# Optimization experiments

Hardware: AMD Instinct MI355X
Metric: run time of the kernel (lower is better)

The kernel has to match this reference:

```python
import jax, jax.numpy as jnp
import numpy as np

N_TOKENS = 1_000_000
NUM_FEATURES = 128
NUM_CLUSTERS = 64


def setup_inputs() -> dict:
    key = jax.random.key(0)
    kx, kc = jax.random.split(key)
    x = jax.random.normal(kx, (1, N_TOKENS, NUM_FEATURES), dtype=jnp.float32)
    # learned parameter, initialized as torch.randn(num_clusters, num_features)
    cluster_centers = jax.random.normal(kc, (NUM_CLUSTERS, NUM_FEATURES), dtype=jnp.float32)
    return {"x": x, "cluster_centers": cluster_centers}


def reference(x, cluster_centers):
    # x: (1, n, d); cluster_centers: (k, d)
    # O(n*k*d) broadcast intermediate of the original). argmin is identical
    # to argmin over torch.norm since sqrt is monotone.
    x2 = jnp.sum(x * x, axis=-1)                                  # (1, n)
    c2 = jnp.sum(cluster_centers * cluster_centers, axis=-1)      # (k,)
    xc = jnp.einsum('bnd,kd->bnk', x, cluster_centers)            # (1, n, k)
    d2 = x2[..., None] + c2[None, None, :] - 2.0 * xc             # (1, n, k)
    # nearest token index for each cluster (min over the token dim)
    indices = jnp.argmin(d2, axis=1)                              # (1, k)
    # gather the selected token features: (1, k, d)
    selected = x[:, indices[0], :]
    return selected
```

## Files before the change

### kernel.cpp

```cpp
#include <hip/hip_runtime.h>
#include <math.h>

#define NTOK   1000000
#define NFEAT  128
#define NCLUS  64
#define TT     256
#define KC     32
#define XPAD   260
#define NTILES ((NTOK + TT - 1) / TT)

__global__ __launch_bounds__(256, 3)
void cluster_part_kernel(const float* __restrict__ x, const float* __restrict__ cc,
                         float* __restrict__ pv, int* __restrict__ pi)
{
    __shared__ float xs[KC][XPAD];
    __shared__ float cs[KC][NCLUS];
    __shared__ float x2s[TT];
    __shared__ float c2s[NCLUS];

    const int tid = threadIdx.x;
    const int cg  = tid & 7;
    const int tg  = tid >> 3;
    const int l   = tid & 3;
    const int g   = tid >> 2;

    const int  tile = blockIdx.x;
    const long tb   = (long)tile * TT;

    float acc[8][8];
    #pragma unroll
    for (int i = 0; i < 8; ++i)
        #pragma unroll
        for (int j = 0; j < 8; ++j) acc[i][j] = 0.f;

    for (int kc = 0; kc < NFEAT / KC; ++kc) {
        __syncthreads();

        {
            const float* src = cc + (long)g * NFEAT + kc * KC + l * 4;
            float4 a = *(const float4*)(src);
            float4 b = *(const float4*)(src + 16);
            cs[l*4+0][g] = a.x; cs[l*4+1][g] = a.y;
            cs[l*4+2][g] = a.z; cs[l*4+3][g] = a.w;
            cs[16+l*4+0][g] = b.x; cs[16+l*4+1][g] = b.y;
            cs[16+l*4+2][g] = b.z; cs[16+l*4+3][g] = b.w;
            float s = 0.f;
            s = fmaf(a.x, a.x, s); s = fmaf(a.y, a.y, s);
            s = fmaf(a.z, a.z, s); s = fmaf(a.w, a.w, s);
            s = fmaf(b.x, b.x, s); s = fmaf(b.y, b.y, s);
            s = fmaf(b.z, b.z, s); s = fmaf(b.w, b.w, s);
            s += __shfl_xor(s, 1);
            s += __shfl_xor(s, 2);
            if (l == 0) { if (kc == 0) c2s[g] = s; else c2s[g] += s; }
        }

        #pragma unroll
        for (int r = 0; r < 4; ++r) {
            const int  row = r * 64 + g;
            long n = tb + row;
            if (n > NTOK - 1) n = NTOK - 1;
            const float* src = x + n * NFEAT + kc * KC + l * 4;
            float4 a = *(const float4*)(src);
            float4 b = *(const float4*)(src + 16);
            xs[l*4+0][row] = a.x; xs[l*4+1][row] = a.y;
            xs[l*4+2][row] = a.z; xs[l*4+3][row] = a.w;
            xs[16+l*4+0][row] = b.x; xs[16+l*4+1][row] = b.y;
            xs[16+l*4+2][row] = b.z; xs[16+l*4+3][row] = b.w;
            float s = 0.f;
            s = fmaf(a.x, a.x, s); s = fmaf(a.y, a.y, s);
            s = fmaf(a.z, a.z, s); s = fmaf(a.w, a.w, s);
            s = fmaf(b.x, b.x, s); s = fmaf(b.y, b.y, s);
            s = fmaf(b.z, b.z, s); s = fmaf(b.w, b.w, s);
            s += __shfl_xor(s, 1);
            s += __shfl_xor(s, 2);
            if (l == 0) { if (kc == 0) x2s[row] = s; else x2s[row] += s; }
        }
        __syncthreads();

        #pragma unroll 2
        for (int k = 0; k < KC; ++k) {
            float4 xa = *(const float4*)&xs[k][tg * 8];
            float4 xb = *(const float4*)&xs[k][tg * 8 + 4];
            float4 ca = *(const float4*)&cs[k][cg * 8];
            float4 cb = *(const float4*)&cs[k][cg * 8 + 4];
            float xv[8] = {xa.x, xa.y, xa.z, xa.w, xb.x, xb.y, xb.z, xb.w};
            float cv[8] = {ca.x, ca.y, ca.z, ca.w, cb.x, cb.y, cb.z, cb.w};
            #pragma unroll
            for (int i = 0; i < 8; ++i)
                #pragma unroll
                for (int j = 0; j < 8; ++j)
                    acc[i][j] = fmaf(xv[i], cv[j], acc[i][j]);
        }
    }

    float bestv[8]; int besti[8];
    #pragma unroll
    for (int j = 0; j < 8; ++j) { bestv[j] = INFINITY; besti[j] = 0; }

    float c2r[8];
    #pragma unroll
    for (int j = 0; j < 8; ++j) c2r[j] = c2s[cg * 8 + j];

    #pragma unroll
    for (int i = 0; i < 8; ++i) {
        const long n = tb + tg * 8 + i;
        if (n >= NTOK) continue;
        const float x2 = x2s[tg * 8 + i];
        #pragma unroll
        for (int j = 0; j < 8; ++j) {
            float s = (x2 + c2r[j]) - 2.0f * acc[i][j];
            if (s < bestv[j]) { bestv[j] = s; besti[j] = (int)n; }
        }
    }

    __syncthreads();
    float* rv = &xs[0][0];
    int*   ri = (int*)&cs[0][0];
    #pragma unroll
    for (int j = 0; j < 8; ++j) {
        rv[(cg * 8 + j) * 32 + tg] = bestv[j];
        ri[(cg * 8 + j) * 32 + tg] = besti[j];
    }
    __syncthreads();
    if (tid < NCLUS) {
        float bv = rv[tid * 32]; int bi = ri[tid * 32];
        #pragma unroll
        for (int t = 1; t < 32; ++t) {
            float v = rv[tid * 32 + t]; int ii = ri[tid * 32 + t];
            if (v < bv || (v == bv && ii < bi)) { bv = v; bi = ii; }
        }
        pv[(long)tile * NCLUS + tid] = bv;
        pi[(long)tile * NCLUS + tid] = bi;
    }
}

__global__ __launch_bounds__(256)
void cluster_final_kernel(const float* __restrict__ x,
                          const float* __restrict__ pv, const int* __restrict__ pi,
                          float* __restrict__ out)
{
    const int c   = blockIdx.x;
    const int tid = threadIdx.x;
    __shared__ float sv[256];
    __shared__ int   si[256];

    float bv = INFINITY; int bi = 0x7fffffff;
    for (int b = tid; b < NTILES; b += 256) {
        float v = pv[(long)b * NCLUS + c]; int ii = pi[(long)b * NCLUS + c];
        if (v < bv || (v == bv && ii < bi)) { bv = v; bi = ii; }
    }
    sv[tid] = bv; si[tid] = bi;
    __syncthreads();
    for (int s = 128; s > 0; s >>= 1) {
        if (tid < s) {
            float v = sv[tid + s]; int ii = si[tid + s];
            if (v < sv[tid] || (v == sv[tid] && ii < si[tid])) {
                sv[tid] = v; si[tid] = ii;
            }
        }
        __syncthreads();
    }
    const int best = si[0];
    if (tid < NFEAT) out[c * NFEAT + tid] = x[(long)best * NFEAT + tid];
}

extern "C" void kernel_launch(void* const* d_in, const int* in_sizes, int n_in,
                              void* d_out, int out_size, void* d_ws, size_t ws_size,
                              hipStream_t stream) {
    const float* x  = (const float*)d_in[0];
    const float* cc = (const float*)d_in[1];
    float* out = (float*)d_out;

    float* pv = (float*)d_ws;
    int*   pi = (int*)((char*)d_ws + (size_t)NTILES * NCLUS * sizeof(float));

    cluster_part_kernel<<<NTILES, 256, 0, stream>>>(x, cc, pv, pi);
    cluster_final_kernel<<<NCLUS, 256, 0, stream>>>(x, pv, pi, out);
}
```

Before: 778.7 us.

## Use persistent blocks with atomic tile scheduler and register-prefetched x chunks

Replaces the one-block-per-tile grid with 768 persistent blocks that pull tiles through an atomic counter, so all 128 centroid features are loaded into shared memory once per block rather than once per tile. x is loaded in 16-feature chunks, with the next chunk prefetched into registers while the current one is computed, which overlaps global loads with the FMA loop. Per-block best values are kept in registers across tiles, which shrinks the partial-result array the final kernel reads. The costs are an extra launch to zero the counter, one atomic per tile, and more shared memory and registers per block, which may lower occupancy.

```diff
diff --git a/kernel.cpp b/kernel.cpp
--- a/kernel.cpp
+++ b/kernel.cpp
@@ -5,18 +5,24 @@
 #define NFEAT  128
 #define NCLUS  64
 #define TT     256
-#define KC     32
+#define KC     16
+#define NCHUNK (NFEAT / KC)
 #define XPAD   260
 #define NTILES ((NTOK + TT - 1) / TT)
+#define GRID_P 768
+
+__global__ void zero_ctr_kernel(int* ctr) { *ctr = 0; }
 
 __global__ __launch_bounds__(256, 3)
 void cluster_part_kernel(const float* __restrict__ x, const float* __restrict__ cc,
+                         int* __restrict__ ctr,
                          float* __restrict__ pv, int* __restrict__ pi)
 {
+    __shared__ float cs[NFEAT][NCLUS];
     __shared__ float xs[KC][XPAD];
-    __shared__ float cs[KC][NCLUS];
     __shared__ float x2s[TT];
     __shared__ float c2s[NCLUS];
+    __shared__ int   tileno;
 
     const int tid = threadIdx.x;
     const int cg  = tid & 7;
@@ -24,98 +30,120 @@
     const int l   = tid & 3;
     const int g   = tid >> 2;
 
-    const int  tile = blockIdx.x;
-    const long tb   = (long)tile * TT;
-
-    float acc[8][8];
-    #pragma unroll
-    for (int i = 0; i < 8; ++i)
-        #pragma unroll
-        for (int j = 0; j < 8; ++j) acc[i][j] = 0.f;
-
-    for (int kc = 0; kc < NFEAT / KC; ++kc) {
-        __syncthreads();
-
-        {
-            const float* src = cc + (long)g * NFEAT + kc * KC + l * 4;
-            float4 a = *(const float4*)(src);
-            float4 b = *(const float4*)(src + 16);
-            cs[l*4+0][g] = a.x; cs[l*4+1][g] = a.y;
-            cs[l*4+2][g] = a.z; cs[l*4+3][g] = a.w;
-            cs[16+l*4+0][g] = b.x; cs[16+l*4+1][g] = b.y;
-            cs[16+l*4+2][g] = b.z; cs[16+l*4+3][g] = b.w;
-            float s = 0.f;
-            s = fmaf(a.x, a.x, s); s = fmaf(a.y, a.y, s);
-            s = fmaf(a.z, a.z, s); s = fmaf(a.w, a.w, s);
-            s = fmaf(b.x, b.x, s); s = fmaf(b.y, b.y, s);
-            s = fmaf(b.z, b.z, s); s = fmaf(b.w, b.w, s);
-            s += __shfl_xor(s, 1);
-            s += __shfl_xor(s, 2);
-            if (l == 0) { if (kc == 0) c2s[g] = s; else c2s[g] += s; }
-        }
-
-        #pragma unroll
-        for (int r = 0; r < 4; ++r) {
-            const int  row = r * 64 + g;
-            long n = tb + row;
-            if (n > NTOK - 1) n = NTOK - 1;
-            const float* src = x + n * NFEAT + kc * KC + l * 4;
-            float4 a = *(const float4*)(src);
-            float4 b = *(const float4*)(src + 16);
-            xs[l*4+0][row] = a.x; xs[l*4+1][row] = a.y;
-            xs[l*4+2][row] = a.z; xs[l*4+3][row] = a.w;
-            xs[16+l*4+0][row] = b.x; xs[16+l*4+1][row] = b.y;
-            xs[16+l*4+2][row] = b.z; xs[16+l*4+3][row] = b.w;
-            float s = 0.f;
-            s = fmaf(a.x, a.x, s); s = fmaf(a.y, a.y, s);
-            s = fmaf(a.z, a.z, s); s = fmaf(a.w, a.w, s);
-            s = fmaf(b.x, b.x, s); s = fmaf(b.y, b.y, s);
-            s = fmaf(b.z, b.z, s); s = fmaf(b.w, b.w, s);
-            s += __shfl_xor(s, 1);
-            s += __shfl_xor(s, 2);
-            if (l == 0) { if (kc == 0) x2s[row] = s; else x2s[row] += s; }
-        }
-        __syncthreads();
-
-        #pragma unroll 2
-        for (int k = 0; k < KC; ++k) {
-            float4 xa = *(const float4*)&xs[k][tg * 8];
-            float4 xb = *(const float4*)&xs[k][tg * 8 + 4];
-            float4 ca = *(const float4*)&cs[k][cg * 8];
-            float4 cb = *(const float4*)&cs[k][cg * 8 + 4];
-            float xv[8] = {xa.x, xa.y, xa.z, xa.w, xb.x, xb.y, xb.z, xb.w};
-            float cv[8] = {ca.x, ca.y, ca.z, ca.w, cb.x, cb.y, cb.z, cb.w};
-            #pragma unroll
-            for (int i = 0; i < 8; ++i)
-                #pragma unroll
-                for (int j = 0; j < 8; ++j)
-                    acc[i][j] = fmaf(xv[i], cv[j], acc[i][j]);
-        }
-    }
-
-    float bestv[8]; int besti[8];
-    #pragma unroll
-    for (int j = 0; j < 8; ++j) { bestv[j] = INFINITY; besti[j] = 0; }
+    {
+        float s = 0.f;
+        const float* src = cc + (long)g * NFEAT + l * 4;
+        #pragma unroll
+        for (int r = 0; r < 8; ++r) {
+            float4 v = *(const float4*)(src + r * 16);
+            const int f = r * 16 + l * 4;
+            cs[f + 0][g] = v.x; cs[f + 1][g] = v.y;
+            cs[f + 2][g] = v.z; cs[f + 3][g] = v.w;
+            s = fmaf(v.x, v.x, s); s = fmaf(v.y, v.y, s);
+            s = fmaf(v.z, v.z, s); s = fmaf(v.w, v.w, s);
+        }
+        s += __shfl_xor(s, 1);
+        s += __shfl_xor(s, 2);
+        if (l == 0) c2s[g] = s;
+    }
+    __syncthreads();
 
     float c2r[8];
     #pragma unroll
     for (int j = 0; j < 8; ++j) c2r[j] = c2s[cg * 8 + j];
 
+    float bestv[8]; int besti[8];
     #pragma unroll
-    for (int i = 0; i < 8; ++i) {
-        const long n = tb + tg * 8 + i;
-        if (n >= NTOK) continue;
-        const float x2 = x2s[tg * 8 + i];
-        #pragma unroll
-        for (int j = 0; j < 8; ++j) {
-            float s = (x2 + c2r[j]) - 2.0f * acc[i][j];
-            if (s < bestv[j]) { bestv[j] = s; besti[j] = (int)n; }
+    for (int j = 0; j < 8; ++j) { bestv[j] = INFINITY; besti[j] = 0x7fffffff; }
+
+    for (;;) {
+        if (tid == 0) tileno = atomicAdd(ctr, 1);
+        __syncthreads();
+        const int tile = tileno;
+        if (tile >= NTILES) break;
+        const long tb = (long)tile * TT;
+
+        float4 pf[4];
+        #pragma unroll
+        for (int r = 0; r < 4; ++r) {
+            long n = tb + r * 64 + g;
+            if (n >= NTOK) n = NTOK - 1;
+            pf[r] = *(const float4*)(x + n * NFEAT + l * 4);
+        }
+
+        float acc[8][8];
+        #pragma unroll
+        for (int i = 0; i < 8; ++i)
+            #pragma unroll
+            for (int j = 0; j < 8; ++j) acc[i][j] = 0.f;
+        float x2a[4] = {0.f, 0.f, 0.f, 0.f};
+
+        #pragma unroll 1
+        for (int kc = 0; kc < NCHUNK; ++kc) {
+            __syncthreads();
+            #pragma unroll
+            for (int r = 0; r < 4; ++r) {
+                float4 v = pf[r];
+                const int row = r * 64 + g;
+                xs[l * 4 + 0][row] = v.x; xs[l * 4 + 1][row] = v.y;
+                xs[l * 4 + 2][row] = v.z; xs[l * 4 + 3][row] = v.w;
+                x2a[r] = fmaf(v.x, v.x, x2a[r]);
+                x2a[r] = fmaf(v.y, v.y, x2a[r]);
+                x2a[r] = fmaf(v.z, v.z, x2a[r]);
+                x2a[r] = fmaf(v.w, v.w, x2a[r]);
+            }
+            if (kc + 1 < NCHUNK) {
+                #pragma unroll
+                for (int r = 0; r < 4; ++r) {
+                    long n = tb + r * 64 + g;
+                    if (n >= NTOK) n = NTOK - 1;
+                    pf[r] = *(const float4*)(x + n * NFEAT + (kc + 1) * KC + l * 4);
+                }
+            }
+            __syncthreads();
+
+            const int kb = kc * KC;
+            #pragma unroll 4
+            for (int k = 0; k < KC; ++k) {
+                float4 xa = *(const float4*)&xs[k][tg * 8];
+                float4 xb = *(const float4*)&xs[k][tg * 8 + 4];
+                float4 ca = *(const float4*)&cs[kb + k][cg * 8];
+                float4 cb = *(const float4*)&cs[kb + k][cg * 8 + 4];
+                float xv[8] = {xa.x, xa.y, xa.z, xa.w, xb.x, xb.y, xb.z, xb.w};
+                float cv[8] = {ca.x, ca.y, ca.z, ca.w, cb.x, cb.y, cb.z, cb.w};
+                #pragma unroll
+                for (int i = 0; i < 8; ++i)
+                    #pragma unroll
+                    for (int j = 0; j < 8; ++j)
+                        acc[i][j] = fmaf(xv[i], cv[j], acc[i][j]);
+            }
+        }
+
+        #pragma unroll
+        for (int r = 0; r < 4; ++r) {
+            float s = x2a[r];
+            s += __shfl_xor(s, 1);
+            s += __shfl_xor(s, 2);
+            if (l == 0) x2s[r * 64 + g] = s;
+        }
+        __syncthreads();
+
+        #pragma unroll
+        for (int i = 0; i < 8; ++i) {
+            const long n = tb + tg * 8 + i;
+            if (n >= NTOK) continue;
+            const float x2 = x2s[tg * 8 + i];
+            #pragma unroll
+            for (int j = 0; j < 8; ++j) {
+                float s = (x2 + c2r[j]) - 2.0f * acc[i][j];
+                if (s < bestv[j]) { bestv[j] = s; besti[j] = (int)n; }
+            }
         }
     }
 
     __syncthreads();
     float* rv = &xs[0][0];
-    int*   ri = (int*)&cs[0][0];
+    int*   ri = (int*)(&xs[0][0] + 2048);
     #pragma unroll
     for (int j = 0; j < 8; ++j) {
         rv[(cg * 8 + j) * 32 + tg] = bestv[j];
@@ -129,8 +157,8 @@
             float v = rv[tid * 32 + t]; int ii = ri[tid * 32 + t];
             if (v < bv || (v == bv && ii < bi)) { bv = v; bi = ii; }
         }
-        pv[(long)tile * NCLUS + tid] = bv;
-        pi[(long)tile * NCLUS + tid] = bi;
+        pv[(long)blockIdx.x * NCLUS + tid] = bv;
+        pi[(long)blockIdx.x * NCLUS + tid] = bi;
     }
 }
 
@@ -145,7 +173,7 @@
     __shared__ int   si[256];
 
     float bv = INFINITY; int bi = 0x7fffffff;
-    for (int b = tid; b < NTILES; b += 256) {
+    for (int b = tid; b < GRID_P; b += 256) {
         float v = pv[(long)b * NCLUS + c]; int ii = pi[(long)b * NCLUS + c];
         if (v < bv || (v == bv && ii < bi)) { bv = v; bi = ii; }
     }
@@ -171,9 +199,11 @@
     const float* cc = (const float*)d_in[1];
     float* out = (float*)d_out;
 
-    float* pv = (float*)d_ws;
-    int*   pi = (int*)((char*)d_ws + (size_t)NTILES * NCLUS * sizeof(float));
-
-    cluster_part_kernel<<<NTILES, 256, 0, stream>>>(x, cc, pv, pi);
+    int*   ctr = (int*)d_ws;
+    float* pv  = (float*)((char*)d_ws + 256);
+    int*   pi  = (int*)((char*)d_ws + 256 + (size_t)GRID_P * NCLUS * sizeof(float));
+
+    zero_ctr_kernel<<<1, 1, 0, stream>>>(ctr);
+    cluster_part_kernel<<<GRID_P, 256, 0, stream>>>(x, cc, ctr, pv, pi);
     cluster_final_kernel<<<NCLUS, 256, 0, stream>>>(x, pv, pi, out);
 }
```

Result: faster. 728.2 us (-6.5%).
